# Optimization experiments

Measured on AMD Instinct MI355X. Metric: run time of the kernel, lower is better.

## Reference

```python
import jax, jax.numpy as jnp
import numpy as np
from jax import lax

V, E, H, B, S, L, T = 30000, 300, 256, 32, 256, 4, 9
H2 = 2 * H            # bidirectional encoder output / decoder hidden
DIN = 2 * H2 + L      # decoder LSTM input size


def setup_inputs() -> dict:
    key = jax.random.key(0)
    ks = jax.random.split(key, 14)
    rn = lambda k, shp, s=0.05: (jax.random.normal(k, shp, dtype=jnp.float32) * s)
    return {
        "seqs": jax.random.randint(ks[0], (B, S), 0, V, dtype=jnp.int32),
        "emb": rn(ks[1], (V, E)),
        "enc_Wih_f": rn(ks[2], (4 * H, E)),
        "enc_Whh_f": rn(ks[3], (4 * H, H)),
        "enc_b_f": rn(ks[4], (4 * H,)),
        "enc_Wih_b": rn(ks[5], (4 * H, E)),
        "enc_Whh_b": rn(ks[6], (4 * H, H)),
        "enc_b_b": rn(ks[7], (4 * H,)),
        "W_att": rn(ks[8], (H2, H2)),
        "dec_Wih": rn(ks[9], (4 * H2, DIN)),
        "dec_Whh": rn(ks[10], (4 * H2, H2)),
        "dec_b": rn(ks[11], (4 * H2,)),
        "W_tag": rn(ks[12], (T, H2)),
        "b_tag": rn(ks[13], (T,)),
    }


def _lstm_scan(x_seq, Wih, Whh, b, hidden):
    """x_seq: [S,B,Din] -> outputs [S,B,hidden]. PyTorch gate order i,f,g,o."""
    nb = x_seq.shape[1]
    h0 = jnp.zeros((nb, hidden), x_seq.dtype)
    c0 = jnp.zeros((nb, hidden), x_seq.dtype)

    def step(carry, x):
        h, c = carry
        g = x @ Wih.T + h @ Whh.T + b
        i, f, gg, o = jnp.split(g, 4, axis=-1)
        c = jax.nn.sigmoid(f) * c + jax.nn.sigmoid(i) * jnp.tanh(gg)
        h = jax.nn.sigmoid(o) * jnp.tanh(c)
        return (h, c), h

    _, hs = lax.scan(step, (h0, c0), x_seq)
    return hs


def reference(seqs, emb, enc_Wih_f, enc_Whh_f, enc_b_f, enc_Wih_b, enc_Whh_b,
              enc_b_b, W_att, dec_Wih, dec_Whh, dec_b, W_tag, b_tag):
    # embed and transpose to [S, B, E]
    x = jnp.transpose(emb[seqs], (1, 0, 2))
    # bidirectional encoder LSTM -> h: [S, B, 2H]
    h_f = _lstm_scan(x, enc_Wih_f, enc_Whh_f, enc_b_f, H)
    h_b = jnp.flip(_lstm_scan(jnp.flip(x, 0), enc_Wih_b, enc_Whh_b, enc_b_b, H), 0)
    h = jnp.concatenate([h_f, h_b], axis=-1)

    # precompute W_att @ h (same math as per-step linear in original)
    Wh = jnp.einsum('sbh,oh->sbo', h, W_att)   # [S,B,H2]

    s0 = jnp.zeros((B, H2), x.dtype)
    c0 = jnp.zeros((B, H2), x.dtype)

    def decode_level(carry, onehot):           # onehot: [L]
        def step(carry2, h_t):                 # h_t: [B,H2]
            s, c = carry2
            score = jnp.einsum('sbo,bo->bs', Wh, s)       # [B,S]
            att = jax.nn.softmax(score, axis=1)
            ctx = jnp.einsum('sbh,bs->bh', h, att)        # [B,H2]
            xin = jnp.concatenate(
                [ctx, h_t, jnp.broadcast_to(onehot, (B, L))], axis=-1)
            g = xin @ dec_Wih.T + s @ dec_Whh.T + dec_b
            i, f, gg, o = jnp.split(g, 4, axis=-1)
            c = jax.nn.sigmoid(f) * c + jax.nn.sigmoid(i) * jnp.tanh(gg)
            s = jax.nn.sigmoid(o) * jnp.tanh(c)
            return (s, c), s

        carry, outs = lax.scan(step, carry, h)  # outs: [S,B,H2]
        return carry, outs

    # state (s,c) persists across nested levels, matching the original loop
    _, all_outs = lax.scan(decode_level, (s0, c0), jnp.eye(L, dtype=x.dtype))
    # [L,S,B,H2] -> tag scores [L,S,B,T]
    return jnp.einsum('lsbh,th->lsbt', all_outs, W_tag) + b_tag
```

## Files before the change

kernel.cpp:

```cpp
#include <hip/hip_runtime.h>
#include <cstdint>
#include <cstddef>

using u16 = unsigned short;
using u32 = unsigned int;

typedef __attribute__((ext_vector_type(8))) __bf16 bf16x8;
typedef __attribute__((ext_vector_type(4))) float f32x4;

__device__ __forceinline__ float bf2f(u16 u){
  union { u32 i; float f; } v; v.i = ((u32)u) << 16; return v.f;
}
__device__ __forceinline__ u16 f2bf(float f){
  union { float f; u32 i; } v; v.f = f;
  return (u16)((v.i + 0x7FFFu + ((v.i >> 16) & 1u)) >> 16);
}
__device__ __forceinline__ float sigm(float x){ return 1.0f / (1.0f + __expf(-x)); }
__device__ __forceinline__ f32x4 mfma16(bf16x8 a, bf16x8 b, f32x4 c){
  return __builtin_amdgcn_mfma_f32_16x16x32_bf16(a, b, c, 0, 0, 0);
}
__device__ __forceinline__ float ldin(const void* p, size_t i, bool f){
  return f ? ((const float*)p)[i] : bf2f(((const u16*)p)[i]);
}

__device__ __forceinline__ uint4 ldx4_cg(const u16* p){
  uint4 r;
  asm volatile("global_load_dwordx4 %0, %1, off sc0 sc1" : "=v"(r) : "v"(p) : "memory");
  return r;
}
__device__ __forceinline__ void st16_cg(u16* p, u32 v){
  asm volatile("global_store_short %0, %1, off sc0 sc1" :: "v"(p), "v"(v) : "memory");
}
__device__ __forceinline__ void wait_vm0(){ asm volatile("s_waitcnt vmcnt(0)" ::: "memory"); }

__device__ __forceinline__ void bar_arrive(u32* bar){
  __hip_atomic_fetch_add(bar, 1u, __ATOMIC_RELAXED, __HIP_MEMORY_SCOPE_AGENT);
}
__device__ __forceinline__ void bar_spin(u32* bar, u32 tgt){
  while (__hip_atomic_load(bar, __ATOMIC_RELAXED, __HIP_MEMORY_SCOPE_AGENT) < tgt)
    __builtin_amdgcn_s_sleep(1);
}

__global__ __launch_bounds__(256) void k_detect(const u32* __restrict__ embw, u32* __restrict__ dflag){
  int tid = threadIdx.x;
  u32 cnt = 0;
  for (int t = 0; t < 32; ++t){
    u32 w = embw[t*256 + tid];
    u32 e = (w >> 7) & 0xFFu;
    cnt += (e >= 0xC0u) ? 1u : 0u;
  }
  atomicAdd(dflag, cnt);
}


__global__ __launch_bounds__(256) void k_pack(
  const void* eWihF, const void* eWihB, const void* ebF, const void* ebB,
  const void* dWih, const void* dWhh, const void* db, const void* Wtag,
  const void* eWhhF, const void* eWhhB, const void* Watt, const void* btag,
  const u32* __restrict__ dflag,
  u16* __restrict__ WihCat, float* __restrict__ bcat, u16* __restrict__ WihH,
  u16* __restrict__ Wf, float* __restrict__ lbv, u16* __restrict__ WtagP,
  u16* __restrict__ WhhFb, u16* __restrict__ WhhBb, u16* __restrict__ Wattb,
  float* __restrict__ btagf)
{
  bool isf = (*dflag > 64u);
  long i = (long)blockIdx.x * 256 + threadIdx.x;
  if (i < 655360){
    long n = i / 320, e = i - n*320;
    WihCat[i] = (e < 300)
      ? f2bf(ldin(n < 1024 ? eWihF : eWihB, (size_t)(n & 1023)*300 + e, isf)) : (u16)0;
    return;
  }
  i -= 655360;
  if (i < 2048){ bcat[i] = ldin(i < 1024 ? ebF : ebB, (size_t)(i & 1023), isf); return; }
  i -= 2048;
  if (i < 1048576){
    long n = i >> 9, k = i & 511;
    WihH[i] = f2bf(ldin(dWih, (size_t)n*1028 + 512 + k, isf));
    return;
  }
  i -= 1048576;
  if (i < 2097152){
    long e  = i & 7;
    long ln = (i >> 3) & 63;
    long kt = (i >> 9) & 31;
    long rt = (i >> 14) & 3;
    long wgi = i >> 16;
    long n = rt*512 + wgi*16 + (ln & 15);
    long k = kt*32 + (ln >> 4)*8 + e;
    Wf[i] = f2bf((k < 512) ? ldin(dWih, (size_t)n*1028 + k, isf)
                           : ldin(dWhh, (size_t)n*512 + (k - 512), isf));
    return;
  }
  i -= 2097152;
  if (i < 8192){
    long l = i >> 11, n = i & 2047;
    lbv[i] = ldin(db, n, isf) + ldin(dWih, (size_t)n*1028 + 1024 + l, isf);
    return;
  }
  i -= 8192;
  if (i < 8192){
    long n = i >> 9, k = i & 511;
    WtagP[i] = (n < 9) ? f2bf(ldin(Wtag, (size_t)n*512 + k, isf)) : (u16)0;
    return;
  }
  i -= 8192;
  if (i < 262144){ WhhFb[i] = f2bf(ldin(eWhhF, i, isf)); return; }
  i -= 262144;
  if (i < 262144){ WhhBb[i] = f2bf(ldin(eWhhB, i, isf)); return; }
  i -= 262144;
  if (i < 262144){ Wattb[i] = f2bf(ldin(Watt, i, isf)); return; }
  i -= 262144;
  if (i < 16){ btagf[i] = (i < 9) ? ldin(btag, i, isf) : 0.f; return; }
}

__global__ __launch_bounds__(256) void k_gather(
  const int* __restrict__ seqs, const void* __restrict__ emb,
  const u32* __restrict__ dflag, u16* __restrict__ X)
{
  bool isf = (*dflag > 64u);
  int idx = blockIdx.x * 256 + threadIdx.x;
  if (idx >= 8192*320) return;
  int row = idx / 320, e = idx - row*320;
  int s = row >> 5, b = row & 31;
  int tok = seqs[b*256 + s];
  X[idx] = (e < 300) ? f2bf(ldin(emb, (size_t)tok*300 + e, isf)) : (u16)0;
}


__global__ __launch_bounds__(256) void k_gemm(
  const u16* __restrict__ A, const u16* __restrict__ B, const float* __restrict__ bias,
  u16* __restrict__ C, int M, int N, int K)
{
  int mb = blockIdx.x * 32;
  int wave = threadIdx.x >> 6, lane = threadIdx.x & 63;
  int nb = blockIdx.y * 256 + wave * 64;
  int rlo = lane & 15, klane = (lane >> 4) * 8;
  f32x4 acc[2][4];
  #pragma unroll
  for (int i = 0; i < 2; ++i)
    #pragma unroll
    for (int j = 0; j < 4; ++j) acc[i][j] = (f32x4){0,0,0,0};
  for (int kk = 0; kk < K; kk += 32){
    bf16x8 a0 = *(const bf16x8*)(A + (size_t)(mb + rlo)*K + kk + klane);
    bf16x8 a1 = *(const bf16x8*)(A + (size_t)(mb + 16 + rlo)*K + kk + klane);
    #pragma unroll
    for (int nt = 0; nt < 4; ++nt){
      bf16x8 bv = *(const bf16x8*)(B + (size_t)(nb + nt*16 + rlo)*K + kk + klane);
      acc[0][nt] = mfma16(a0, bv, acc[0][nt]);
      acc[1][nt] = mfma16(a1, bv, acc[1][nt]);
    }
  }
  int rbase = (lane >> 4) * 4;
  #pragma unroll
  for (int mt = 0; mt < 2; ++mt)
    #pragma unroll
    for (int nt = 0; nt < 4; ++nt){
      int col = nb + nt*16 + rlo;
      float badd = bias ? bias[col] : 0.0f;
      #pragma unroll
      for (int r = 0; r < 4; ++r){
        int row = mb + mt*16 + rbase + r;
        C[(size_t)row*N + col] = f2bf(acc[mt][nt][r] + badd);
      }
    }
}


__global__ __launch_bounds__(256) void k_transp(const u16* __restrict__ hglob, u16* __restrict__ hT)
{
  __shared__ u16 tile_t[64][264];
  int b = blockIdx.x >> 3, d0 = (blockIdx.x & 7) * 64;
  int t = threadIdx.x;
  for (int rr = 0; rr < 16; ++rr){
    int c = rr*256 + t;
    int j = c >> 4, dq = (c & 15) * 4;
    ushort4 ld = *(const ushort4*)(hglob + ((size_t)(j*32 + b)*512 + d0 + dq));
    tile_t[dq + 0][j] = ld.x;
    tile_t[dq + 1][j] = ld.y;
    tile_t[dq + 2][j] = ld.z;
    tile_t[dq + 3][j] = ld.w;
  }
  __syncthreads();
  for (int rr = 0; rr < 8; ++rr){
    int c = rr*256 + t;
    int d = c >> 5, jq = (c & 31) * 8;
    *(uint4*)(hT + ((size_t)(b*512 + d0 + d)*256 + jq)) = *(const uint4*)&tile_t[d][jq];
  }
}


__global__ __launch_bounds__(256, 1) void k_encoder(
  const u16* __restrict__ XW, const u16* __restrict__ WhhF, const u16* __restrict__ WhhB,
  u16* __restrict__ hglob, u16* __restrict__ hstate, u32* ctrl)
{
  int wg = blockIdx.x;
  int d = wg >> 4, w = wg & 15;
  const u16* Whh = d ? WhhB : WhhF;
  u32* bar = ctrl + d * 64;
  int tid = threadIdx.x, wave = tid >> 6, lane = tid & 63;
  int cc = lane & 15, q = lane >> 4, klane = q * 8, rbase = q * 4;
  __shared__ __align__(16) u16 hblk[8192];
  __shared__ float g_lds[4][32][16];
  __shared__ float c_sh[512];
  c_sh[tid] = 0.f; c_sh[tid + 256] = 0.f;
  __syncthreads();

  for (int t = 0; t < 256; ++t){
    int srow = d ? (255 - t) : t;
    const u16* hr = hstate + (size_t)(d*2 + (t & 1)) * 8192;
    u16*       hw = hstate + (size_t)(d*2 + ((t & 1) ^ 1)) * 8192;

    {
      int c0 = tid, c1 = tid + 256, c2 = tid + 512, c3 = tid + 768;
      uint4 v0 = ldx4_cg(hr + (c0 >> 5)*256 + (c0 & 31)*8);
      uint4 v1 = ldx4_cg(hr + (c1 >> 5)*256 + (c1 & 31)*8);
      uint4 v2 = ldx4_cg(hr + (c2 >> 5)*256 + (c2 & 31)*8);
      uint4 v3 = ldx4_cg(hr + (c3 >> 5)*256 + (c3 & 31)*8);
      wait_vm0();
      *(uint4*)(hblk + (c0 >> 5)*256 + (((c0 & 31) ^ ((c0 >> 5) & 7)))*8) = v0;
      *(uint4*)(hblk + (c1 >> 5)*256 + (((c1 & 31) ^ ((c1 >> 5) & 7)))*8) = v1;
      *(uint4*)(hblk + (c2 >> 5)*256 + (((c2 & 31) ^ ((c2 >> 5) & 7)))*8) = v2;
      *(uint4*)(hblk + (c3 >> 5)*256 + (((c3 & 31) ^ ((c3 >> 5) & 7)))*8) = v3;
    }
    __syncthreads();

    {
      int ncol = wave*256 + w*16 + cc;
      const u16* Brow = Whh + (size_t)ncol*256;
      f32x4 acc0 = {0,0,0,0}, acc1 = {0,0,0,0};
      #pragma unroll
      for (int kt = 0; kt < 8; ++kt){
        bf16x8 bv = *(const bf16x8*)(Brow + kt*32 + klane);
        bf16x8 a0 = *(const bf16x8*)(hblk + cc*256 + ((kt*4 + q) ^ (cc & 7))*8);
        bf16x8 a1 = *(const bf16x8*)(hblk + (cc + 16)*256 + ((kt*4 + q) ^ (cc & 7))*8);
        acc0 = mfma16(a0, bv, acc0);
        acc1 = mfma16(a1, bv, acc1);
      }
      #pragma unroll
      for (int r = 0; r < 4; ++r){
        g_lds[wave][rbase + r][cc]      = acc0[r];
        g_lds[wave][16 + rbase + r][cc] = acc1[r];
      }
    }
    __syncthreads();

    for (int e = tid; e < 512; e += 256){
      int b_ = e >> 4, jc = e & 15;
      int j = w*16 + jc;
      float pre[4];
      #pragma unroll
      for (int g2 = 0; g2 < 4; ++g2)
        pre[g2] = g_lds[g2][b_][jc] + bf2f(XW[(size_t)(srow*32 + b_)*2048 + d*1024 + g2*256 + j]);
      float iv = sigm(pre[0]), fv = sigm(pre[1]);
      float gv = tanhf(pre[2]), ov = sigm(pre[3]);
      float cv = fv * c_sh[e] + iv * gv;
      c_sh[e] = cv;
      u16 hb = f2bf(ov * tanhf(cv));
      st16_cg(hw + b_*256 + j, (u32)hb);
      __builtin_nontemporal_store(hb, hglob + (size_t)(srow*32 + b_)*512 + d*256 + j);
    }
    wait_vm0();
    __syncthreads();
    if (tid == 0){
      bar_arrive(bar);
      bar_spin(bar, (u32)(t + 1) * 16u);
    }
    __syncthreads();
  }
}


__global__ __launch_bounds__(512, 1) void k_decoder(
  const u16* __restrict__ Whb, const u16* __restrict__ hT,
  const u16* __restrict__ Wf, const u16* __restrict__ Xh, const float* __restrict__ lbv,
  u16* __restrict__ Ain,
  u16* __restrict__ aouts,
  u32* bar1, u32* bar2)
{
  extern __shared__ __align__(16) u16 ablk[];
  __shared__ float score_lds[256];
  __shared__ __align__(16) u16 att_bf[256];
  __shared__ float gbuf[4][16][33];
  __shared__ float c_lds[512];
  const int wg = blockIdx.x, tid = threadIdx.x;
  const int wave = tid >> 6, lane = tid & 63;
  const int q = lane >> 4, cc = lane & 15;
  c_lds[tid] = 0.0f;

  bf16x8 wh[2][16];
  #pragma unroll
  for (int rt = 0; rt < 2; ++rt)
    #pragma unroll
    for (int kt = 0; kt < 16; ++kt){
      int row = wave*32 + rt*16 + cc;
      wh[rt][kt] = *(const bf16x8*)(Whb + ((size_t)(row*32 + wg))*512 + kt*32 + q*8);
    }
  const int grt = wave >> 1, gct = wave & 1;
  const int bcol = gct*16 + cc;
  const u16* WfW = Wf + (size_t)wg*65536;
  __syncthreads();

  for (int iter = 0; iter < 1024; ++iter){
    const int l = iter >> 8, t = iter & 255;
    u16* AinC = Ain + (iter & 1)*32768;
    u16* AinN = Ain + ((iter & 1) ^ 1)*32768;

    {
      int c0 = tid, c1 = tid + 512, c2 = tid + 1024, c3 = tid + 1536;
      uint4 v0 = ldx4_cg(AinC + (c0 >> 6)*1024 + 512 + (c0 & 63)*8);
      uint4 v1 = ldx4_cg(AinC + (c1 >> 6)*1024 + 512 + (c1 & 63)*8);
      uint4 v2 = ldx4_cg(AinC + (c2 >> 6)*1024 + 512 + (c2 & 63)*8);
      uint4 v3 = ldx4_cg(AinC + (c3 >> 6)*1024 + 512 + (c3 & 63)*8);
      wait_vm0();
      *(uint4*)(ablk + (c0 >> 6)*1024 + (64 + ((c0 & 63) ^ ((c0 >> 6) & 7)))*8) = v0;
      *(uint4*)(ablk + (c1 >> 6)*1024 + (64 + ((c1 & 63) ^ ((c1 >> 6) & 7)))*8) = v1;
      *(uint4*)(ablk + (c2 >> 6)*1024 + (64 + ((c2 & 63) ^ ((c2 >> 6) & 7)))*8) = v2;
      *(uint4*)(ablk + (c3 >> 6)*1024 + (64 + ((c3 & 63) ^ ((c3 >> 6) & 7)))*8) = v3;
    }
    __syncthreads();

    f32x4 sa0 = {0,0,0,0}, sa1 = {0,0,0,0};
    #pragma unroll
    for (int kt = 0; kt < 16; ++kt){
      bf16x8 sv = *(const bf16x8*)(ablk + wg*1024 + ((64 + kt*4 + q) ^ (wg & 7))*8);
      sa0 = mfma16(wh[0][kt], sv, sa0);
      sa1 = mfma16(wh[1][kt], sv, sa1);
    }
    if (cc == 0){
      #pragma unroll
      for (int r = 0; r < 4; ++r){
        score_lds[wave*32      + q*4 + r] = sa0[r];
        score_lds[wave*32 + 16 + q*4 + r] = sa1[r];
      }
    }
    __syncthreads();

    if (wave == 0){
      float x0 = score_lds[lane*4+0], x1 = score_lds[lane*4+1];
      float x2 = score_lds[lane*4+2], x3 = score_lds[lane*4+3];
      float m = fmaxf(fmaxf(x0,x1), fmaxf(x2,x3));
      #pragma unroll
      for (int off = 32; off >= 1; off >>= 1) m = fmaxf(m, __shfl_xor(m, off));
      float e0 = __expf(x0-m), e1 = __expf(x1-m), e2 = __expf(x2-m), e3 = __expf(x3-m);
      float s = e0+e1+e2+e3;
      #pragma unroll
      for (int off = 32; off >= 1; off >>= 1) s += __shfl_xor(s, off);
      float inv = 1.0f / s;
      att_bf[lane*4+0] = f2bf(e0*inv);
      att_bf[lane*4+1] = f2bf(e1*inv);
      att_bf[lane*4+2] = f2bf(e2*inv);
      att_bf[lane*4+3] = f2bf(e3*inv);
    }
    __syncthreads();

    f32x4 ca0 = {0,0,0,0}, ca1 = {0,0,0,0}, ca2 = {0,0,0,0}, ca3 = {0,0,0,0};
    #pragma unroll
    for (int jt = 0; jt < 8; ++jt){
      uint4 au = {0,0,0,0};
      if (cc == 0) au = *(const uint4*)(att_bf + jt*32 + q*8);
      bf16x8 af = *(bf16x8*)&au;
      const u16* hb = hT + ((size_t)(wg*512 + wave*64 + cc))*256 + jt*32 + q*8;
      ca0 = mfma16(af, *(const bf16x8*)(hb +  0*256), ca0);
      ca1 = mfma16(af, *(const bf16x8*)(hb + 16*256), ca1);
      ca2 = mfma16(af, *(const bf16x8*)(hb + 32*256), ca2);
      ca3 = mfma16(af, *(const bf16x8*)(hb + 48*256), ca3);
    }
    if (q == 0){
      u16* dst = AinC + wg*1024 + wave*64 + cc;
      st16_cg(dst +  0, (u32)f2bf(ca0[0]));
      st16_cg(dst + 16, (u32)f2bf(ca1[0]));
      st16_cg(dst + 32, (u32)f2bf(ca2[0]));
      st16_cg(dst + 48, (u32)f2bf(ca3[0]));
    }
    wait_vm0();
    __syncthreads();
    if (tid == 0) bar_arrive(bar2);

    f32x4 ga = {0,0,0,0};
    #pragma unroll
    for (int kt = 16; kt < 32; ++kt){
      bf16x8 wa = *(const bf16x8*)(WfW + ((grt*32 + kt)*64 + lane)*8);
      bf16x8 av = *(const bf16x8*)(ablk + bcol*1024 + ((kt*4 + q) ^ (bcol & 7))*8);
      ga = mfma16(wa, av, ga);
    }
    if (tid == 0) bar_spin(bar2, 32u*(u32)(iter+1));
    __syncthreads();

    {
      int c0 = tid, c1 = tid + 512, c2 = tid + 1024, c3 = tid + 1536;
      uint4 v0 = ldx4_cg(AinC + (c0 >> 6)*1024 + (c0 & 63)*8);
      uint4 v1 = ldx4_cg(AinC + (c1 >> 6)*1024 + (c1 & 63)*8);
      uint4 v2 = ldx4_cg(AinC + (c2 >> 6)*1024 + (c2 & 63)*8);
      uint4 v3 = ldx4_cg(AinC + (c3 >> 6)*1024 + (c3 & 63)*8);
      wait_vm0();
      *(uint4*)(ablk + (c0 >> 6)*1024 + (((c0 & 63) ^ ((c0 >> 6) & 7)))*8) = v0;
      *(uint4*)(ablk + (c1 >> 6)*1024 + (((c1 & 63) ^ ((c1 >> 6) & 7)))*8) = v1;
      *(uint4*)(ablk + (c2 >> 6)*1024 + (((c2 & 63) ^ ((c2 >> 6) & 7)))*8) = v2;
      *(uint4*)(ablk + (c3 >> 6)*1024 + (((c3 & 63) ^ ((c3 >> 6) & 7)))*8) = v3;
    }
    __syncthreads();

    #pragma unroll
    for (int kt = 0; kt < 16; ++kt){
      bf16x8 wa = *(const bf16x8*)(WfW + ((grt*32 + kt)*64 + lane)*8);
      bf16x8 av = *(const bf16x8*)(ablk + bcol*1024 + ((kt*4 + q) ^ (bcol & 7))*8);
      ga = mfma16(wa, av, ga);
    }
    #pragma unroll
    for (int r = 0; r < 4; ++r) gbuf[grt][q*4 + r][bcol] = ga[r];
    __syncthreads();

    {
      const int b_ = tid >> 4, dd = tid & 15;
      const int gj = wg*16 + dd;
      float pre[4];
      #pragma unroll
      for (int g = 0; g < 4; ++g){
        int n = g*512 + gj;
        pre[g] = gbuf[g][dd][b_] + bf2f(Xh[(size_t)(t*32 + b_)*2048 + n]) + lbv[l*2048 + n];
      }
      float iv = sigm(pre[0]), fv = sigm(pre[1]);
      float gv = tanhf(pre[2]), ov = sigm(pre[3]);
      float cv = fv * c_lds[tid] + iv * gv;
      c_lds[tid] = cv;
      u16 hb = f2bf(ov * tanhf(cv));
      st16_cg(AinN + b_*1024 + 512 + gj, (u32)hb);
      __builtin_nontemporal_store(hb, aouts + (size_t)((l*256 + t)*32 + b_)*512 + gj);
    }
    wait_vm0();
    __syncthreads();
    if (tid == 0){
      bar_arrive(bar1);
      bar_spin(bar1, 32u*(u32)(iter+1));
    }
    __syncthreads();
  }
}


__global__ __launch_bounds__(256) void k_tag(
  const u16* __restrict__ aouts, const u16* __restrict__ WtagP, const float* __restrict__ btagf,
  const u32* __restrict__ dflag, void* __restrict__ out)
{
  bool isf = (*dflag > 64u);
  int wave = threadIdx.x >> 6, lane = threadIdx.x & 63;
  int mb = (blockIdx.x * 4 + wave) * 16;
  int cc = lane & 15, klane = (lane >> 4) * 8;
  f32x4 acc = {0,0,0,0};
  const u16* Arow = aouts + (size_t)(mb + cc)*512;
  const u16* Brow = WtagP + cc*512;
  #pragma unroll
  for (int kk = 0; kk < 512; kk += 32){
    bf16x8 av = *(const bf16x8*)(Arow + kk + klane);
    bf16x8 bv = *(const bf16x8*)(Brow + kk + klane);
    acc = mfma16(av, bv, acc);
  }
  int rbase = (lane >> 4) * 4;
  if (cc < 9){
    float bt = btagf[cc];
    #pragma unroll
    for (int r = 0; r < 4; ++r){
      int row = mb + rbase + r;
      float v = acc[r] + bt;
      if (isf) ((float*)out)[(size_t)row*9 + cc] = v;
      else     ((u16*)out)[(size_t)row*9 + cc] = f2bf(v);
    }
  }
}


extern "C" void kernel_launch(void* const* d_in, const int* in_sizes, int n_in,
                              void* d_out, int out_size, void* d_ws, size_t ws_size,
                              hipStream_t stream)
{
  (void)in_sizes; (void)n_in; (void)out_size;
  if (ws_size < 98625536ull) return;

  const int* seqs = (const int*)d_in[0];

  char* ws = (char*)d_ws;
  u32*    ctrl   = (u32*)(ws + 0);
  u32*    dflag  = ctrl + 240;
  u16*    Ain    = (u16*)(ws + 1024);
  u16*    hstate = (u16*)(ws + 132096);
  u16*    WihCat = (u16*)(ws + 263168);
  float*  bcat   = (float*)(ws + 1573888);
  u16*    WihH   = (u16*)(ws + 1582080);
  u16*    Wf     = (u16*)(ws + 3679232);
  float*  lbv    = (float*)(ws + 7873536);
  u16*    WtagP  = (u16*)(ws + 7906304);
  u16*    WhhFb  = (u16*)(ws + 7922688);
  u16*    WhhBb  = (u16*)(ws + 8446976);
  u16*    Wattb  = (u16*)(ws + 8971264);
  float*  btagf  = (float*)(ws + 9495552);
  u16*    X      = (u16*)(ws + 9496576);
  u16*    XWXh   = (u16*)(ws + 14739456);
  u16*    aouts  = (u16*)(ws + 48293888);
  u16*    hglob  = (u16*)(ws + 48293888);
  u16*    hT     = (u16*)(ws + 81848320);
  u16*    Whb    = (u16*)(ws + 90236928);

  hipMemsetAsync(d_ws, 0, 263168, stream);

  k_detect<<<1, 256, 0, stream>>>((const u32*)d_in[1], dflag);
  k_pack<<<17993, 256, 0, stream>>>(
      d_in[2], d_in[5], d_in[4], d_in[7], d_in[9], d_in[10], d_in[11], d_in[12],
      d_in[3], d_in[6], d_in[8], d_in[13], dflag,
      WihCat, bcat, WihH, Wf, lbv, WtagP, WhhFb, WhhBb, Wattb, btagf);
  k_gather<<<10240, 256, 0, stream>>>(seqs, d_in[1], dflag, X);
  k_gemm<<<dim3(256, 8), 256, 0, stream>>>(X, WihCat, bcat, XWXh, 8192, 2048, 320);
  k_encoder<<<32, 256, 0, stream>>>(XWXh, WhhFb, WhhBb, hglob, hstate, ctrl);
  k_gemm<<<dim3(256, 2), 256, 0, stream>>>(hglob, Wattb, nullptr, Whb, 8192, 512, 512);
  k_gemm<<<dim3(256, 8), 256, 0, stream>>>(hglob, WihH, nullptr, XWXh, 8192, 2048, 512);
  k_transp<<<256, 256, 0, stream>>>(hglob, hT);

  k_decoder<<<32, 512, 65536, stream>>>(Whb, hT, Wf, XWXh, lbv, Ain, aouts,
                                        ctrl + 128, ctrl + 160);
  k_tag<<<512, 256, 0, stream>>>(aouts, WtagP, btagf, dflag, d_out);
}
```

Measured before the change: 21.52 ms.

## Replace atomic grid barriers with per-block flags and halve decoder block count

Swaps the atomic counter grid barriers in the encoder and decoder for per-block progress flags. Each block writes its own flag, and one wave polls all 16 flags with coherent loads. The decoder now runs as 16 blocks of 1024 threads instead of 32 of 512, each handling two batch rows and 32 hidden columns. The attention Wh matrix is reordered by the GEMM so rows are read straight from global memory instead of being held in registers. The Xh and bias loads are hoisted before the recurrent dependency. This targets per-step grid synchronisation latency in the long sequential decode loop, at the cost of more global Wh reads per step and heavier blocks.

```diff
diff --git a/kernel.cpp b/kernel.cpp
--- a/kernel.cpp
+++ b/kernel.cpp
@@ -28,17 +28,30 @@
   asm volatile("global_load_dwordx4 %0, %1, off sc0 sc1" : "=v"(r) : "v"(p) : "memory");
   return r;
 }
+__device__ __forceinline__ u32 ld32_cg(const u32* p){
+  u32 r;
+  asm volatile("global_load_dword %0, %1, off sc0 sc1" : "=v"(r) : "v"(p) : "memory");
+  return r;
+}
 __device__ __forceinline__ void st16_cg(u16* p, u32 v){
   asm volatile("global_store_short %0, %1, off sc0 sc1" :: "v"(p), "v"(v) : "memory");
 }
+__device__ __forceinline__ void st32_cg(u32* p, u32 v){
+  asm volatile("global_store_dword %0, %1, off sc0 sc1" :: "v"(p), "v"(v) : "memory");
+}
 __device__ __forceinline__ void wait_vm0(){ asm volatile("s_waitcnt vmcnt(0)" ::: "memory"); }
 
-__device__ __forceinline__ void bar_arrive(u32* bar){
-  __hip_atomic_fetch_add(bar, 1u, __ATOMIC_RELAXED, __HIP_MEMORY_SCOPE_AGENT);
-}
-__device__ __forceinline__ void bar_spin(u32* bar, u32 tgt){
-  while (__hip_atomic_load(bar, __ATOMIC_RELAXED, __HIP_MEMORY_SCOPE_AGENT) < tgt)
-    __builtin_amdgcn_s_sleep(1);
+__device__ __forceinline__ void wait_flags16(const u32* f, u32 tgt){
+  if (threadIdx.x < 64){
+    const u32* p = f + (threadIdx.x & 15);
+    for (;;){
+      u32 v = ld32_cg(p);
+      wait_vm0();
+      if (__all((int)(v >= tgt))) break;
+      __builtin_amdgcn_s_sleep(2);
+    }
+  }
+  __syncthreads();
 }
 
 __global__ __launch_bounds__(256) void k_detect(const u32* __restrict__ embw, u32* __restrict__ dflag){
@@ -81,12 +94,13 @@
   }
   i -= 1048576;
   if (i < 2097152){
-    long e  = i & 7;
-    long ln = (i >> 3) & 63;
-    long kt = (i >> 9) & 31;
-    long rt = (i >> 14) & 3;
-    long wgi = i >> 16;
-    long n = rt*512 + wgi*16 + (ln & 15);
+    long e   = i & 7;
+    long ln  = (i >> 3) & 63;
+    long kt  = (i >> 9) & 31;
+    long dh  = (i >> 14) & 1;
+    long grt = (i >> 15) & 3;
+    long wgi = i >> 17;
+    long n = grt*512 + wgi*32 + dh*16 + (ln & 15);
     long k = kt*32 + (ln >> 4)*8 + e;
     Wf[i] = f2bf((k < 512) ? ldin(dWih, (size_t)n*1028 + k, isf)
                            : ldin(dWhh, (size_t)n*512 + (k - 512), isf));
@@ -130,7 +144,7 @@
 
 __global__ __launch_bounds__(256) void k_gemm(
   const u16* __restrict__ A, const u16* __restrict__ B, const float* __restrict__ bias,
-  u16* __restrict__ C, int M, int N, int K)
+  u16* __restrict__ C, int M, int N, int K, int perm)
 {
   int mb = blockIdx.x * 32;
   int wave = threadIdx.x >> 6, lane = threadIdx.x & 63;
@@ -161,7 +175,8 @@
       #pragma unroll
       for (int r = 0; r < 4; ++r){
         int row = mb + mt*16 + rbase + r;
-        C[(size_t)row*N + col] = f2bf(acc[mt][nt][r] + badd);
+        int crow = perm ? ((row & 31)*256 + (row >> 5)) : row;
+        C[(size_t)crow*N + col] = f2bf(acc[mt][nt][r] + badd);
       }
     }
 }
@@ -192,12 +207,12 @@
 
 __global__ __launch_bounds__(256, 1) void k_encoder(
   const u16* __restrict__ XW, const u16* __restrict__ WhhF, const u16* __restrict__ WhhB,
-  u16* __restrict__ hglob, u16* __restrict__ hstate, u32* ctrl)
+  u16* __restrict__ hglob, u16* __restrict__ hstate, u32* ctrlE)
 {
   int wg = blockIdx.x;
   int d = wg >> 4, w = wg & 15;
   const u16* Whh = d ? WhhB : WhhF;
-  u32* bar = ctrl + d * 64;
+  u32* fE = ctrlE + d * 32;
   int tid = threadIdx.x, wave = tid >> 6, lane = tid & 63;
   int cc = lane & 15, q = lane >> 4, klane = q * 8, rbase = q * 4;
   __shared__ __align__(16) u16 hblk[8192];
@@ -210,6 +225,8 @@
     int srow = d ? (255 - t) : t;
     const u16* hr = hstate + (size_t)(d*2 + (t & 1)) * 8192;
     u16*       hw = hstate + (size_t)(d*2 + ((t & 1) ^ 1)) * 8192;
+
+    if (t > 0) wait_flags16(fE, (u32)t);
 
     {
       int c0 = tid, c1 = tid + 256, c2 = tid + 512, c3 = tid + 768;
@@ -262,83 +279,86 @@
     }
     wait_vm0();
     __syncthreads();
-    if (tid == 0){
-      bar_arrive(bar);
-      bar_spin(bar, (u32)(t + 1) * 16u);
-    }
-    __syncthreads();
-  }
-}
-
-
-__global__ __launch_bounds__(512, 1) void k_decoder(
-  const u16* __restrict__ Whb, const u16* __restrict__ hT,
+    if (tid == 0) st32_cg(fE + w, (u32)(t + 1));
+  }
+}
+
+
+__global__ __launch_bounds__(1024, 1) void k_decoder(
+  const u16* __restrict__ Whp, const u16* __restrict__ hT,
   const u16* __restrict__ Wf, const u16* __restrict__ Xh, const float* __restrict__ lbv,
   u16* __restrict__ Ain,
   u16* __restrict__ aouts,
-  u32* bar1, u32* bar2)
+  u32* fS, u32* fC)
 {
   extern __shared__ __align__(16) u16 ablk[];
-  __shared__ float score_lds[256];
-  __shared__ __align__(16) u16 att_bf[256];
-  __shared__ float gbuf[4][16][33];
-  __shared__ float c_lds[512];
+  __shared__ float score_lds[512];
+  __shared__ __align__(16) u16 att_bf[512];
+  __shared__ float gbuf[4][32][33];
+  __shared__ float c_lds[1024];
   const int wg = blockIdx.x, tid = threadIdx.x;
   const int wave = tid >> 6, lane = tid & 63;
   const int q = lane >> 4, cc = lane & 15;
+  const int bb = wave >> 3, aw = wave & 7;
+  const int batt = wg*2 + bb;
+  const int grt = wave >> 2, sub = wave & 3;
+  const int gct = sub >> 1, dh = sub & 1;
+  const int bcol = gct*16 + cc;
+  const u16* WfW = Wf + (size_t)wg*131072;
+  const int pb_ = tid >> 5, pdd = tid & 31;
+  const int pgj = wg*32 + pdd;
   c_lds[tid] = 0.0f;
-
-  bf16x8 wh[2][16];
-  #pragma unroll
-  for (int rt = 0; rt < 2; ++rt)
-    #pragma unroll
-    for (int kt = 0; kt < 16; ++kt){
-      int row = wave*32 + rt*16 + cc;
-      wh[rt][kt] = *(const bf16x8*)(Whb + ((size_t)(row*32 + wg))*512 + kt*32 + q*8);
-    }
-  const int grt = wave >> 1, gct = wave & 1;
-  const int bcol = gct*16 + cc;
-  const u16* WfW = Wf + (size_t)wg*65536;
-  __syncthreads();
+  float lb[4];
 
   for (int iter = 0; iter < 1024; ++iter){
     const int l = iter >> 8, t = iter & 255;
     u16* AinC = Ain + (iter & 1)*32768;
     u16* AinN = Ain + ((iter & 1) ^ 1)*32768;
 
-    {
-      int c0 = tid, c1 = tid + 512, c2 = tid + 1024, c3 = tid + 1536;
+    if (iter > 0) wait_flags16(fS, (u32)iter);
+
+    {
+      int c0 = tid, c1 = tid + 1024;
       uint4 v0 = ldx4_cg(AinC + (c0 >> 6)*1024 + 512 + (c0 & 63)*8);
       uint4 v1 = ldx4_cg(AinC + (c1 >> 6)*1024 + 512 + (c1 & 63)*8);
-      uint4 v2 = ldx4_cg(AinC + (c2 >> 6)*1024 + 512 + (c2 & 63)*8);
-      uint4 v3 = ldx4_cg(AinC + (c3 >> 6)*1024 + 512 + (c3 & 63)*8);
       wait_vm0();
       *(uint4*)(ablk + (c0 >> 6)*1024 + (64 + ((c0 & 63) ^ ((c0 >> 6) & 7)))*8) = v0;
       *(uint4*)(ablk + (c1 >> 6)*1024 + (64 + ((c1 & 63) ^ ((c1 >> 6) & 7)))*8) = v1;
-      *(uint4*)(ablk + (c2 >> 6)*1024 + (64 + ((c2 & 63) ^ ((c2 >> 6) & 7)))*8) = v2;
-      *(uint4*)(ablk + (c3 >> 6)*1024 + (64 + ((c3 & 63) ^ ((c3 >> 6) & 7)))*8) = v3;
-    }
-    __syncthreads();
-
-    f32x4 sa0 = {0,0,0,0}, sa1 = {0,0,0,0};
-    #pragma unroll
-    for (int kt = 0; kt < 16; ++kt){
-      bf16x8 sv = *(const bf16x8*)(ablk + wg*1024 + ((64 + kt*4 + q) ^ (wg & 7))*8);
-      sa0 = mfma16(wh[0][kt], sv, sa0);
-      sa1 = mfma16(wh[1][kt], sv, sa1);
-    }
-    if (cc == 0){
-      #pragma unroll
-      for (int r = 0; r < 4; ++r){
-        score_lds[wave*32      + q*4 + r] = sa0[r];
-        score_lds[wave*32 + 16 + q*4 + r] = sa1[r];
-      }
-    }
-    __syncthreads();
-
-    if (wave == 0){
-      float x0 = score_lds[lane*4+0], x1 = score_lds[lane*4+1];
-      float x2 = score_lds[lane*4+2], x3 = score_lds[lane*4+3];
+    }
+    __syncthreads();
+
+    if ((iter & 255) == 0){
+      #pragma unroll
+      for (int g = 0; g < 4; ++g) lb[g] = lbv[l*2048 + g*512 + pgj];
+    }
+    float xh[4];
+    #pragma unroll
+    for (int g = 0; g < 4; ++g) xh[g] = bf2f(Xh[(size_t)(t*32 + pb_)*2048 + g*512 + pgj]);
+
+    {
+      f32x4 sa0 = {0,0,0,0}, sa1 = {0,0,0,0};
+      const u16* WhRow = Whp + ((size_t)(batt*256 + aw*32 + cc))*512;
+      #pragma unroll
+      for (int kt = 0; kt < 16; ++kt){
+        bf16x8 sv = *(const bf16x8*)(ablk + batt*1024 + ((64 + kt*4 + q) ^ (batt & 7))*8);
+        bf16x8 w0 = *(const bf16x8*)(WhRow + kt*32 + q*8);
+        bf16x8 w1 = *(const bf16x8*)(WhRow + 16*512 + kt*32 + q*8);
+        sa0 = mfma16(w0, sv, sa0);
+        sa1 = mfma16(w1, sv, sa1);
+      }
+      if (cc == 0){
+        #pragma unroll
+        for (int r = 0; r < 4; ++r){
+          score_lds[bb*256 + aw*32      + q*4 + r] = sa0[r];
+          score_lds[bb*256 + aw*32 + 16 + q*4 + r] = sa1[r];
+        }
+      }
+    }
+    __syncthreads();
+
+    if (aw == 0){
+      float x0 = score_lds[bb*256 + lane*4+0], x1 = score_lds[bb*256 + lane*4+1];
+      float x2 = score_lds[bb*256 + lane*4+2], x3 = score_lds[bb*256 + lane*4+3];
       float m = fmaxf(fmaxf(x0,x1), fmaxf(x2,x3));
       #pragma unroll
       for (int off = 32; off >= 1; off >>= 1) m = fmaxf(m, __shfl_xor(m, off));
@@ -347,94 +367,83 @@
       #pragma unroll
       for (int off = 32; off >= 1; off >>= 1) s += __shfl_xor(s, off);
       float inv = 1.0f / s;
-      att_bf[lane*4+0] = f2bf(e0*inv);
-      att_bf[lane*4+1] = f2bf(e1*inv);
-      att_bf[lane*4+2] = f2bf(e2*inv);
-      att_bf[lane*4+3] = f2bf(e3*inv);
-    }
-    __syncthreads();
-
-    f32x4 ca0 = {0,0,0,0}, ca1 = {0,0,0,0}, ca2 = {0,0,0,0}, ca3 = {0,0,0,0};
-    #pragma unroll
-    for (int jt = 0; jt < 8; ++jt){
-      uint4 au = {0,0,0,0};
-      if (cc == 0) au = *(const uint4*)(att_bf + jt*32 + q*8);
-      bf16x8 af = *(bf16x8*)&au;
-      const u16* hb = hT + ((size_t)(wg*512 + wave*64 + cc))*256 + jt*32 + q*8;
-      ca0 = mfma16(af, *(const bf16x8*)(hb +  0*256), ca0);
-      ca1 = mfma16(af, *(const bf16x8*)(hb + 16*256), ca1);
-      ca2 = mfma16(af, *(const bf16x8*)(hb + 32*256), ca2);
-      ca3 = mfma16(af, *(const bf16x8*)(hb + 48*256), ca3);
-    }
-    if (q == 0){
-      u16* dst = AinC + wg*1024 + wave*64 + cc;
-      st16_cg(dst +  0, (u32)f2bf(ca0[0]));
-      st16_cg(dst + 16, (u32)f2bf(ca1[0]));
-      st16_cg(dst + 32, (u32)f2bf(ca2[0]));
-      st16_cg(dst + 48, (u32)f2bf(ca3[0]));
+      att_bf[bb*256 + lane*4+0] = f2bf(e0*inv);
+      att_bf[bb*256 + lane*4+1] = f2bf(e1*inv);
+      att_bf[bb*256 + lane*4+2] = f2bf(e2*inv);
+      att_bf[bb*256 + lane*4+3] = f2bf(e3*inv);
+    }
+    __syncthreads();
+
+    {
+      f32x4 ca0 = {0,0,0,0}, ca1 = {0,0,0,0}, ca2 = {0,0,0,0}, ca3 = {0,0,0,0};
+      #pragma unroll
+      for (int jt = 0; jt < 8; ++jt){
+        uint4 au = {0,0,0,0};
+        if (cc == 0) au = *(const uint4*)(att_bf + bb*256 + jt*32 + q*8);
+        bf16x8 af = *(bf16x8*)&au;
+        const u16* hb = hT + ((size_t)(batt*512 + aw*64 + cc))*256 + jt*32 + q*8;
+        ca0 = mfma16(af, *(const bf16x8*)(hb +  0*256), ca0);
+        ca1 = mfma16(af, *(const bf16x8*)(hb + 16*256), ca1);
+        ca2 = mfma16(af, *(const bf16x8*)(hb + 32*256), ca2);
+        ca3 = mfma16(af, *(const bf16x8*)(hb + 48*256), ca3);
+      }
+      if (q == 0){
+        u16* dst = AinC + batt*1024 + aw*64 + cc;
+        st16_cg(dst +  0, (u32)f2bf(ca0[0]));
+        st16_cg(dst + 16, (u32)f2bf(ca1[0]));
+        st16_cg(dst + 32, (u32)f2bf(ca2[0]));
+        st16_cg(dst + 48, (u32)f2bf(ca3[0]));
+      }
     }
     wait_vm0();
     __syncthreads();
-    if (tid == 0) bar_arrive(bar2);
+    if (tid == 0) st32_cg(fC + wg, (u32)(iter + 1));
 
     f32x4 ga = {0,0,0,0};
     #pragma unroll
     for (int kt = 16; kt < 32; ++kt){
-      bf16x8 wa = *(const bf16x8*)(WfW + ((grt*32 + kt)*64 + lane)*8);
+      bf16x8 wa = *(const bf16x8*)(WfW + (((grt*2 + dh)*32 + kt)*64 + lane)*8);
       bf16x8 av = *(const bf16x8*)(ablk + bcol*1024 + ((kt*4 + q) ^ (bcol & 7))*8);
       ga = mfma16(wa, av, ga);
     }
-    if (tid == 0) bar_spin(bar2, 32u*(u32)(iter+1));
-    __syncthreads();
-
-    {
-      int c0 = tid, c1 = tid + 512, c2 = tid + 1024, c3 = tid + 1536;
+    wait_flags16(fC, (u32)(iter + 1));
+
+    {
+      int c0 = tid, c1 = tid + 1024;
       uint4 v0 = ldx4_cg(AinC + (c0 >> 6)*1024 + (c0 & 63)*8);
       uint4 v1 = ldx4_cg(AinC + (c1 >> 6)*1024 + (c1 & 63)*8);
-      uint4 v2 = ldx4_cg(AinC + (c2 >> 6)*1024 + (c2 & 63)*8);
-      uint4 v3 = ldx4_cg(AinC + (c3 >> 6)*1024 + (c3 & 63)*8);
       wait_vm0();
       *(uint4*)(ablk + (c0 >> 6)*1024 + (((c0 & 63) ^ ((c0 >> 6) & 7)))*8) = v0;
       *(uint4*)(ablk + (c1 >> 6)*1024 + (((c1 & 63) ^ ((c1 >> 6) & 7)))*8) = v1;
-      *(uint4*)(ablk + (c2 >> 6)*1024 + (((c2 & 63) ^ ((c2 >> 6) & 7)))*8) = v2;
-      *(uint4*)(ablk + (c3 >> 6)*1024 + (((c3 & 63) ^ ((c3 >> 6) & 7)))*8) = v3;
     }
     __syncthreads();
 
     #pragma unroll
     for (int kt = 0; kt < 16; ++kt){
-      bf16x8 wa = *(const bf16x8*)(WfW + ((grt*32 + kt)*64 + lane)*8);
+      bf16x8 wa = *(const bf16x8*)(WfW + (((grt*2 + dh)*32 + kt)*64 + lane)*8);
       bf16x8 av = *(const bf16x8*)(ablk + bcol*1024 + ((kt*4 + q) ^ (bcol & 7))*8);
       ga = mfma16(wa, av, ga);
     }
     #pragma unroll
-    for (int r = 0; r < 4; ++r) gbuf[grt][q*4 + r][bcol] = ga[r];
-    __syncthreads();
-
-    {
-      const int b_ = tid >> 4, dd = tid & 15;
-      const int gj = wg*16 + dd;
+    for (int r = 0; r < 4; ++r) gbuf[grt][dh*16 + q*4 + r][bcol] = ga[r];
+    __syncthreads();
+
+    {
       float pre[4];
       #pragma unroll
-      for (int g = 0; g < 4; ++g){
-        int n = g*512 + gj;
-        pre[g] = gbuf[g][dd][b_] + bf2f(Xh[(size_t)(t*32 + b_)*2048 + n]) + lbv[l*2048 + n];
-      }
+      for (int g = 0; g < 4; ++g)
+        pre[g] = gbuf[g][pdd][pb_] + xh[g] + lb[g];
       float iv = sigm(pre[0]), fv = sigm(pre[1]);
       float gv = tanhf(pre[2]), ov = sigm(pre[3]);
       float cv = fv * c_lds[tid] + iv * gv;
       c_lds[tid] = cv;
       u16 hb = f2bf(ov * tanhf(cv));
-      st16_cg(AinN + b_*1024 + 512 + gj, (u32)hb);
-      __builtin_nontemporal_store(hb, aouts + (size_t)((l*256 + t)*32 + b_)*512 + gj);
+      st16_cg(AinN + pb_*1024 + 512 + pgj, (u32)hb);
+      __builtin_nontemporal_store(hb, aouts + (size_t)((l*256 + t)*32 + pb_)*512 + pgj);
     }
     wait_vm0();
     __syncthreads();
-    if (tid == 0){
-      bar_arrive(bar1);
-      bar_spin(bar1, 32u*(u32)(iter+1));
-    }
-    __syncthreads();
+    if (tid == 0) st32_cg(fS + wg, (u32)(iter + 1));
   }
 }
 
@@ -480,8 +489,10 @@
   const int* seqs = (const int*)d_in[0];
 
   char* ws = (char*)d_ws;
-  u32*    ctrl   = (u32*)(ws + 0);
-  u32*    dflag  = ctrl + 240;
+  u32*    fS     = (u32*)(ws + 0);
+  u32*    fC     = (u32*)(ws + 128);
+  u32*    ctrlE  = (u32*)(ws + 256);
+  u32*    dflag  = (u32*)(ws + 512);
   u16*    Ain    = (u16*)(ws + 1024);
   u16*    hstate = (u16*)(ws + 132096);
   u16*    WihCat = (u16*)(ws + 263168);
@@ -499,7 +510,7 @@
   u16*    aouts  = (u16*)(ws + 48293888);
   u16*    hglob  = (u16*)(ws + 48293888);
   u16*    hT     = (u16*)(ws + 81848320);
-  u16*    Whb    = (u16*)(ws + 90236928);
+  u16*    Whp    = (u16*)(ws + 90236928);
 
   hipMemsetAsync(d_ws, 0, 263168, stream);
 
@@ -509,13 +520,12 @@
       d_in[3], d_in[6], d_in[8], d_in[13], dflag,
       WihCat, bcat, WihH, Wf, lbv, WtagP, WhhFb, WhhBb, Wattb, btagf);
   k_gather<<<10240, 256, 0, stream>>>(seqs, d_in[1], dflag, X);
-  k_gemm<<<dim3(256, 8), 256, 0, stream>>>(X, WihCat, bcat, XWXh, 8192, 2048, 320);
-  k_encoder<<<32, 256, 0, stream>>>(XWXh, WhhFb, WhhBb, hglob, hstate, ctrl);
-  k_gemm<<<dim3(256, 2), 256, 0, stream>>>(hglob, Wattb, nullptr, Whb, 8192, 512, 512);
-  k_gemm<<<dim3(256, 8), 256, 0, stream>>>(hglob, WihH, nullptr, XWXh, 8192, 2048, 512);
+  k_gemm<<<dim3(256, 8), 256, 0, stream>>>(X, WihCat, bcat, XWXh, 8192, 2048, 320, 0);
+  k_encoder<<<32, 256, 0, stream>>>(XWXh, WhhFb, WhhBb, hglob, hstate, ctrlE);
+  k_gemm<<<dim3(256, 2), 256, 0, stream>>>(hglob, Wattb, nullptr, Whp, 8192, 512, 512, 1);
+  k_gemm<<<dim3(256, 8), 256, 0, stream>>>(hglob, WihH, nullptr, XWXh, 8192, 2048, 512, 0);
   k_transp<<<256, 256, 0, stream>>>(hglob, hT);
 
-  k_decoder<<<32, 512, 65536, stream>>>(Whb, hT, Wf, XWXh, lbv, Ain, aouts,
-                                        ctrl + 128, ctrl + 160);
+  k_decoder<<<16, 1024, 65536, stream>>>(Whp, hT, Wf, XWXh, lbv, Ain, aouts, fS, fC);
   k_tag<<<512, 256, 0, stream>>>(aouts, WtagP, btagf, dflag, d_out);
 }
```

New measurement: 48.06 ms. +123.3%, slower.
